# Performance work log

Hardware: AMD Instinct MI355X
Metric: run time of the kernel (lower is better)

## Reference

```python
import jax, jax.numpy as jnp
import numpy as np

B, V, C, A = 32, 48, 24, 6
NC, D, H, OUT = 10000, 128, 128, 167


def setup_inputs() -> dict:
    key = jax.random.key(0)
    ks = jax.random.split(key, 12)
    seqs = jax.random.randint(ks[0], (B, V, C), 0, NC + 1)
    ancestors = jax.random.randint(ks[1], (B, V, C, A), 0, NC + 1)
    length = jax.random.randint(ks[2], (B,), 1, V + 1)
    amask = (jax.random.uniform(ks[3], (B, V, C, A)) < 0.7).astype(jnp.float32)
    amask = amask.at[..., 0].set(1.0)  # first ancestor always valid
    emb = jax.random.normal(ks[4], (NC + 1, D), dtype=jnp.float32) * 0.02
    emb = emb.at[NC].set(0.0)  # padding row is zeros
    w_basic = jax.random.normal(ks[5], (D, 2 * D), dtype=jnp.float32) * (1.0 / np.sqrt(2 * D))
    u_basic_w = jax.random.normal(ks[6], (1, D), dtype=jnp.float32) * (1.0 / np.sqrt(D))
    u_basic_b = jnp.zeros((1,), jnp.float32)
    gru_wih = jax.random.normal(ks[7], (3 * H, D), dtype=jnp.float32) * (1.0 / np.sqrt(H))
    gru_whh = jax.random.normal(ks[8], (3 * H, H), dtype=jnp.float32) * (1.0 / np.sqrt(H))
    gru_bih = jnp.zeros((3 * H,), jnp.float32)
    gru_bhh = jnp.zeros((3 * H,), jnp.float32)
    out_w = jax.random.normal(ks[9], (OUT, H), dtype=jnp.float32) * (1.0 / np.sqrt(H))
    out_b = jnp.zeros((OUT,), jnp.float32)
    return dict(seqs=seqs, ancestors=ancestors, length=length, ancestor_length=amask,
                emb=emb, w_basic=w_basic, u_basic_w=u_basic_w, u_basic_b=u_basic_b,
                gru_wih=gru_wih, gru_whh=gru_whh, gru_bih=gru_bih, gru_bhh=gru_bhh,
                out_w=out_w, out_b=out_b)


def _gram_forward(seqs, ancestors, length, ancestor_length, emb, w_basic,
                  u_basic_w, u_basic_b, gru_wih, gru_whh, gru_bih, gru_bhh,
                  out_w, out_b):
    # gather embeddings
    seqs_e = emb[seqs]            # [B,V,C,D]
    anc_e = emb[ancestors]        # [B,V,C,A,D]
    seqs_rep = jnp.broadcast_to(seqs_e[..., None, :], anc_e.shape)
    # Bahdanau attention: mask applied to concat BEFORE the linear (as in source)
    cat = jnp.concatenate([seqs_rep, anc_e], axis=-1) * ancestor_length[..., None]  # [B,V,C,A,2D]
    hdd = jnp.tanh(jnp.einsum('bvcad,ed->bvcae', cat, w_basic))  # [B,V,C,A,D]
    score = jnp.einsum('bvcad,od->bvcao', hdd, u_basic_w) + u_basic_b  # [B,V,C,A,1]
    # mask_softmax over ancestor axis, faithful to the source (sum==0 -> -1)
    e = jnp.exp(score) * ancestor_length[..., None]
    s = jnp.sum(e, axis=3, keepdims=True)
    s = jnp.where(s == 0, -1.0, s)
    attn = e / s                  # [B,V,C,A,1]
    ctx = jnp.sum(attn * anc_e, axis=3)            # [B,V,C,D] weighted ancestor sum
    x = jnp.tanh(jnp.sum(ctx, axis=2))             # [B,V,D] visit embedding

    # single-layer GRU over visits (valid steps form a prefix, padded tail masked below)
    hsz = gru_whh.shape[1]
    def step(hstate, xt):
        gi = xt @ gru_wih.T + gru_bih              # [B,3H]
        gh = hstate @ gru_whh.T + gru_bhh
        ir, iz, inn = jnp.split(gi, 3, axis=-1)
        hr, hz, hn = jnp.split(gh, 3, axis=-1)
        r = jax.nn.sigmoid(ir + hr)
        z = jax.nn.sigmoid(iz + hz)
        n = jnp.tanh(inn + r * hn)
        hnew = (1.0 - z) * n + z * hstate
        return hnew, hnew
    h0 = jnp.zeros((x.shape[0], hsz), x.dtype)
    _, outs = jax.lax.scan(step, h0, jnp.swapaxes(x, 0, 1))  # [V,B,H]
    outs = jnp.swapaxes(outs, 0, 1)                          # [B,V,H]

    visit_mask = (jnp.arange(x.shape[1])[None, :] < length[:, None]).astype(x.dtype)
    context = jnp.einsum('bv,bvh->bh', visit_mask, outs)     # masked sum over visits
    logit = jax.nn.sigmoid(context @ out_w.T + out_b)        # dropout=eval (identity)
    return logit


def reference(seqs, ancestors, length, ancestor_length, emb, w_basic, u_basic_w,
              u_basic_b, gru_wih, gru_whh, gru_bih, gru_bhh, out_w, out_b):
    return _gram_forward(seqs, ancestors, length, ancestor_length, emb, w_basic,
                         u_basic_w, u_basic_b, gru_wih, gru_whh, gru_bih, gru_bhh,
                         out_w, out_b)
```

## Files before the change

kernel.cpp:

```cpp
#include <hip/hip_runtime.h>

#define BB 32
#define VV 48
#define CC 24
#define AA 6
#define NCODES 10001
#define DD 128
#define HH 128
#define OUTN 167
#define G3 384

typedef float f32x4 __attribute__((ext_vector_type(4)));

__device__ __forceinline__ float fast_tanh(float x) {
    return 1.0f - 2.0f / (1.0f + __expf(2.0f * x));
}
__device__ __forceinline__ float fast_sigmoid(float x) {
    return 1.0f / (1.0f + __expf(-x));
}
__device__ __forceinline__ float dot4(float4 a, float4 b) {
    return a.x * b.x + a.y * b.y + a.z * b.z + a.w * b.w;
}
__device__ __forceinline__ float dot4v(f32x4 a, f32x4 b) {
    return a.x * b.x + a.y * b.y + a.z * b.z + a.w * b.w;
}

__global__ __launch_bounds__(256) void k_precompute(
    const float* __restrict__ emb, const float* __restrict__ w_basic,
    float* __restrict__ P1, float* __restrict__ P2, int nrows)
{
    __shared__ float embs[8][128];
    int row0 = blockIdx.x * 8;
    int t = threadIdx.x;
    for (int i = t; i < 8 * 128; i += 256) {
        int r = i >> 7, d = i & 127;
        int row = row0 + r;
        embs[r][d] = (row < nrows) ? emb[row * 128 + d] : 0.0f;
    }
    __syncthreads();
    int e = t & 127, sel = t >> 7;
    const float* wrow = w_basic + e * 256 + sel * 128;
    float acc[8] = {0, 0, 0, 0, 0, 0, 0, 0};
#pragma unroll 8
    for (int d = 0; d < 128; ++d) {
        float w = wrow[d];
#pragma unroll
        for (int r = 0; r < 8; ++r) acc[r] += embs[r][d] * w;
    }
    float* dst = sel ? P2 : P1;
#pragma unroll
    for (int r = 0; r < 8; ++r) {
        int row = row0 + r;
        if (row < nrows) dst[row * 128 + e] = acc[r];
    }
}

__global__ __launch_bounds__(256) void k_attention(
    const int* __restrict__ seqs, const int* __restrict__ ancestors,
    const float* __restrict__ amask, const float* __restrict__ emb,
    const float* __restrict__ P1, const float* __restrict__ P2,
    const float* __restrict__ u_w, const float* __restrict__ u_b,
    float* __restrict__ x_out)
{
    __shared__ __align__(16) float u_s[128];
    __shared__ float sc_s[144];
    __shared__ float m_s[144];
    __shared__ int   anc_s[144];
    __shared__ float attn_s[144];
    __shared__ float sum_s[24];
    __shared__ float xred[256];
    int bv = blockIdx.x;
    int t = threadIdx.x;
    if (t < 128) u_s[t] = u_w[t];
    __syncthreads();
    float ub = u_b[0];
    int g = t >> 2, l = t & 3;
    for (int p = g; p < CC * AA; p += 64) {
        int c = p / AA, a = p - c * AA;
        int sidx = bv * CC + c;
        int s_code = seqs[sidx];
        int aidx = sidx * AA + a;
        int anc = ancestors[aidx];
        float m = amask[aidx];
        const float4* p14 = (const float4*)(P1 + s_code * 128);
        const float4* p24 = (const float4*)(P2 + anc * 128);
        const float4* u4 = (const float4*)u_s;
        float partial = 0.0f;
        int e4 = l * 8;
#pragma unroll 2
        for (int j = 0; j < 8; ++j) {
            float4 av = p14[e4 + j];
            float4 bv_ = p24[e4 + j];
            float4 uv = u4[e4 + j];
            partial += fast_tanh(m * (av.x + bv_.x)) * uv.x;
            partial += fast_tanh(m * (av.y + bv_.y)) * uv.y;
            partial += fast_tanh(m * (av.z + bv_.z)) * uv.z;
            partial += fast_tanh(m * (av.w + bv_.w)) * uv.w;
        }
        partial += __shfl_xor(partial, 1);
        partial += __shfl_xor(partial, 2);
        if (l == 0) {
            sc_s[p] = partial + ub;
            m_s[p] = m;
            anc_s[p] = anc;
        }
    }
    __syncthreads();
    if (t < CC * AA) attn_s[t] = __expf(sc_s[t]) * m_s[t];
    __syncthreads();
    if (t < CC) {
        float s = 0.0f;
#pragma unroll
        for (int a = 0; a < AA; ++a) s += attn_s[t * AA + a];
        sum_s[t] = (s == 0.0f) ? -1.0f : s;
    }
    __syncthreads();
    if (t < CC * AA) attn_s[t] = attn_s[t] / sum_s[t / AA];
    __syncthreads();
    int e = t & 127, hc = t >> 7;
    float acc = 0.0f;
    for (int c = hc * 12; c < hc * 12 + 12; ++c) {
#pragma unroll
        for (int a = 0; a < AA; ++a) {
            int p = c * AA + a;
            acc += attn_s[p] * emb[anc_s[p] * 128 + e];
        }
    }
    xred[t] = acc;
    __syncthreads();
    if (t < 128) {
        x_out[bv * 128 + t] = fast_tanh(xred[t] + xred[t + 128]);
    }
}

__global__ __launch_bounds__(384, 2) void k_gi(
    const float* __restrict__ x, const float* __restrict__ wih,
    const float* __restrict__ bih, float* __restrict__ gi)
{
    __shared__ __align__(16) float xs[8][128];
    int row0 = blockIdx.x * 8;
    int t = threadIdx.x;
    for (int i = t; i < 8 * 32; i += 384) {
        ((float4*)xs)[i] = ((const float4*)x)[row0 * 32 + i];
    }
    __syncthreads();
    const float4* wrow4 = (const float4*)(wih + t * 128);
    float acc[8] = {0, 0, 0, 0, 0, 0, 0, 0};
#pragma unroll 2
    for (int d4 = 0; d4 < 32; ++d4) {
        float4 wv = wrow4[d4];
#pragma unroll
        for (int r = 0; r < 8; ++r) {
            float4 xv = ((const float4*)xs[r])[d4];
            acc[r] += dot4(xv, wv);
        }
    }
    float bb = bih[t];
#pragma unroll
    for (int r = 0; r < 8; ++r) gi[(row0 + r) * G3 + t] = acc[r] + bb;
}

#define GL4(dst, base, OFF) \
    asm volatile("global_load_dwordx4 %0, %1, off offset:" #OFF \
                 : "=v"(dst) : "v"(base))

__global__ __launch_bounds__(256, 1) void k_gru(
    const float* __restrict__ gi, const float* __restrict__ whh,
    const float* __restrict__ bhh, const int* __restrict__ length,
    const float* __restrict__ out_w, const float* __restrict__ out_b,
    float* __restrict__ out)
{
    __shared__ __align__(16) float hs[2][128];
    __shared__ __align__(16) float ctxs[128];
    int b = blockIdx.x;
    int t = threadIdx.x;
    int o = t >> 1, half = t & 1;

    const f32x4* bwr = (const f32x4*)(whh + o * 128 + half * 64);
    const f32x4* bwz = (const f32x4*)(whh + (128 + o) * 128 + half * 64);
    const f32x4* bwn = (const f32x4*)(whh + (256 + o) * 128 + half * 64);

    f32x4 wr0, wr1, wr2, wr3, wr4, wr5, wr6, wr7,
          wr8, wr9, wr10, wr11, wr12, wr13, wr14, wr15;
    f32x4 wz0, wz1, wz2, wz3, wz4, wz5, wz6, wz7,
          wz8, wz9, wz10, wz11, wz12, wz13, wz14, wz15;
    f32x4 wn0, wn1, wn2, wn3, wn4, wn5, wn6, wn7,
          wn8, wn9, wn10, wn11, wn12, wn13, wn14, wn15;

    GL4(wr0,  bwr, 0);   GL4(wr1,  bwr, 16);  GL4(wr2,  bwr, 32);  GL4(wr3,  bwr, 48);
    GL4(wr4,  bwr, 64);  GL4(wr5,  bwr, 80);  GL4(wr6,  bwr, 96);  GL4(wr7,  bwr, 112);
    GL4(wr8,  bwr, 128); GL4(wr9,  bwr, 144); GL4(wr10, bwr, 160); GL4(wr11, bwr, 176);
    GL4(wr12, bwr, 192); GL4(wr13, bwr, 208); GL4(wr14, bwr, 224); GL4(wr15, bwr, 240);
    GL4(wz0,  bwz, 0);   GL4(wz1,  bwz, 16);  GL4(wz2,  bwz, 32);  GL4(wz3,  bwz, 48);
    GL4(wz4,  bwz, 64);  GL4(wz5,  bwz, 80);  GL4(wz6,  bwz, 96);  GL4(wz7,  bwz, 112);
    GL4(wz8,  bwz, 128); GL4(wz9,  bwz, 144); GL4(wz10, bwz, 160); GL4(wz11, bwz, 176);
    GL4(wz12, bwz, 192); GL4(wz13, bwz, 208); GL4(wz14, bwz, 224); GL4(wz15, bwz, 240);
    GL4(wn0,  bwn, 0);   GL4(wn1,  bwn, 16);  GL4(wn2,  bwn, 32);  GL4(wn3,  bwn, 48);
    GL4(wn4,  bwn, 64);  GL4(wn5,  bwn, 80);  GL4(wn6,  bwn, 96);  GL4(wn7,  bwn, 112);
    GL4(wn8,  bwn, 128); GL4(wn9,  bwn, 144); GL4(wn10, bwn, 160); GL4(wn11, bwn, 176);
    GL4(wn12, bwn, 192); GL4(wn13, bwn, 208); GL4(wn14, bwn, 224); GL4(wn15, bwn, 240);

    float bhr = 0.f, bhz = 0.f, bhn = 0.f;
    if (half == 0) {
        bhr = bhh[o];
        bhz = bhh[128 + o];
        bhn = bhh[256 + o];
    }
    if (t < 128) hs[0][t] = 0.0f;
    int len = length[b];
    float ctx = 0.0f;

    const float* gib = gi + b * VV * G3;
    float aR = 0.f, aZ = 0.f, aN = 0.f;
    float pR = 0.f, pZ = 0.f, pN = 0.f;
    if (half == 0) {
        aR = gib[o];       aZ = gib[128 + o];       aN = gib[256 + o];
        const float* g1 = gib + G3;
        pR = g1[o];        pZ = g1[128 + o];        pN = g1[256 + o];
    }
    asm volatile("s_waitcnt vmcnt(0)" ::: "memory");
    __builtin_amdgcn_sched_barrier(0);
    __syncthreads();

#define STEP2(J, A, B_) do {                                          \
        f32x4 hA = h4[J]; f32x4 hB = h4[J + 1];                       \
        ar0 += dot4v(wr##A, hA);  ar1 += dot4v(wr##B_, hB);           \
        az0 += dot4v(wz##A, hA);  az1 += dot4v(wz##B_, hB);           \
        an0 += dot4v(wn##A, hA);  an1 += dot4v(wn##B_, hB);           \
    } while (0)

    int cur = 0;
    for (int v = 0; v < VV; ++v) {
        float nR = 0.f, nZ = 0.f, nN = 0.f;
        if (half == 0 && v + 2 < VV) {
            const float* g = gib + (v + 2) * G3;
            nR = g[o]; nZ = g[128 + o]; nN = g[256 + o];
        }
        const f32x4* h4 = ((const f32x4*)hs[cur]) + half * 16;
        float ar0 = 0.f, ar1 = 0.f, az0 = 0.f, az1 = 0.f, an0 = 0.f, an1 = 0.f;
        STEP2(0, 0, 1);   STEP2(2, 2, 3);   STEP2(4, 4, 5);   STEP2(6, 6, 7);
        STEP2(8, 8, 9);   STEP2(10, 10, 11); STEP2(12, 12, 13); STEP2(14, 14, 15);
        float ar = ar0 + ar1;
        float az = az0 + az1;
        float an = an0 + an1;
        ar += __shfl_xor(ar, 1);
        az += __shfl_xor(az, 1);
        an += __shfl_xor(an, 1);
        if (half == 0) {
            float r = fast_sigmoid(aR + ar + bhr);
            float z = fast_sigmoid(aZ + az + bhz);
            float n = fast_tanh(aN + r * (an + bhn));
            float hold = hs[cur][o];
            float hnew = (1.0f - z) * n + z * hold;
            hs[cur ^ 1][o] = hnew;
            if (v < len) ctx += hnew;
        }
        aR = pR; aZ = pZ; aN = pN;
        pR = nR; pZ = nZ; pN = nN;
        cur ^= 1;
        __syncthreads();
    }
#undef STEP2

    if (half == 0) ctxs[o] = ctx;
    __syncthreads();
    if (t < OUTN) {
        const float4* w4 = (const float4*)(out_w + t * 128);
        const float4* c4 = (const float4*)ctxs;
        float a0 = 0.f, a1 = 0.f;
#pragma unroll 2
        for (int j = 0; j < 32; j += 2) {
            a0 += dot4(w4[j], c4[j]);
            a1 += dot4(w4[j + 1], c4[j + 1]);
        }
        out[b * OUTN + t] = fast_sigmoid(a0 + a1 + out_b[t]);
    }
}

extern "C" void kernel_launch(void* const* d_in, const int* in_sizes, int n_in,
                              void* d_out, int out_size, void* d_ws, size_t ws_size,
                              hipStream_t stream) {
    const int*   seqs      = (const int*)d_in[0];
    const int*   ancestors = (const int*)d_in[1];
    const int*   length    = (const int*)d_in[2];
    const float* amask     = (const float*)d_in[3];
    const float* emb       = (const float*)d_in[4];
    const float* w_basic   = (const float*)d_in[5];
    const float* u_w       = (const float*)d_in[6];
    const float* u_b       = (const float*)d_in[7];
    const float* wih       = (const float*)d_in[8];
    const float* whh       = (const float*)d_in[9];
    const float* bih       = (const float*)d_in[10];
    const float* bhh       = (const float*)d_in[11];
    const float* out_w     = (const float*)d_in[12];
    const float* out_b     = (const float*)d_in[13];
    float* out = (float*)d_out;

    float* ws = (float*)d_ws;
    float* P1 = ws;
    float* P2 = P1 + NCODES * 128;
    float* x  = P2 + NCODES * 128;
    float* gi = x + BB * VV * 128;

    k_precompute<<<(NCODES + 7) / 8, 256, 0, stream>>>(emb, w_basic, P1, P2, NCODES);
    k_attention<<<BB * VV, 256, 0, stream>>>(seqs, ancestors, amask, emb, P1, P2, u_w, u_b, x);
    k_gi<<<(BB * VV) / 8, 384, 0, stream>>>(x, wih, bih, gi);
    k_gru<<<BB, 256, 0, stream>>>(gi, whh, bhh, length, out_w, out_b, out);
}
```

Baseline: 136.1 us.

## Stage GRU input gates in LDS and pack two batches per GRU block

The GRU kernel now runs two batch rows per 512-thread block and bulk-copies the precomputed input-gate activations into shared memory in two 24-step chunks, replacing the per-step register prefetch from global memory. The k_gi kernel drops its shared-memory staging of x and reads x directly from global, and its occupancy hint is removed. This aims to take global load latency off the serial recurrence, at the cost of 72KB of LDS, a mid-loop reload barrier, and half as many GRU blocks each running twice the threads.

After: 153.7 us. +12.9%, slower.

```diff
diff --git a/kernel.cpp b/kernel.cpp
--- a/kernel.cpp
+++ b/kernel.cpp
@@ -133,26 +133,21 @@
     }
 }
 
-__global__ __launch_bounds__(384, 2) void k_gi(
+__global__ __launch_bounds__(384) void k_gi(
     const float* __restrict__ x, const float* __restrict__ wih,
     const float* __restrict__ bih, float* __restrict__ gi)
 {
-    __shared__ __align__(16) float xs[8][128];
     int row0 = blockIdx.x * 8;
     int t = threadIdx.x;
-    for (int i = t; i < 8 * 32; i += 384) {
-        ((float4*)xs)[i] = ((const float4*)x)[row0 * 32 + i];
-    }
-    __syncthreads();
-    const float4* wrow4 = (const float4*)(wih + t * 128);
-    float acc[8] = {0, 0, 0, 0, 0, 0, 0, 0};
+    const float4* w4 = (const float4*)(wih + t * 128);
+    const float4* x4 = (const float4*)(x + row0 * 128);
+    float acc[8] = {};
 #pragma unroll 2
     for (int d4 = 0; d4 < 32; ++d4) {
-        float4 wv = wrow4[d4];
+        float4 wv = w4[d4];
 #pragma unroll
         for (int r = 0; r < 8; ++r) {
-            float4 xv = ((const float4*)xs[r])[d4];
-            acc[r] += dot4(xv, wv);
+            acc[r] += dot4(x4[r * 32 + d4], wv);
         }
     }
     float bb = bih[t];
@@ -164,17 +159,20 @@
     asm volatile("global_load_dwordx4 %0, %1, off offset:" #OFF \
                  : "=v"(dst) : "v"(base))
 
-__global__ __launch_bounds__(256, 1) void k_gru(
+__global__ __launch_bounds__(512, 1) void k_gru(
     const float* __restrict__ gi, const float* __restrict__ whh,
     const float* __restrict__ bhh, const int* __restrict__ length,
     const float* __restrict__ out_w, const float* __restrict__ out_b,
     float* __restrict__ out)
 {
-    __shared__ __align__(16) float hs[2][128];
-    __shared__ __align__(16) float ctxs[128];
-    int b = blockIdx.x;
+    __shared__ __align__(16) float gl[2][24 * G3];
+    __shared__ __align__(16) float hs[2][2][128];
+    __shared__ __align__(16) float ctxs[2][128];
     int t = threadIdx.x;
-    int o = t >> 1, half = t & 1;
+    int tb = t >> 8;
+    int tt = t & 255;
+    int b = blockIdx.x * 2 + tb;
+    int o = tt >> 1, half = tt & 1;
 
     const f32x4* bwr = (const f32x4*)(whh + o * 128 + half * 64);
     const f32x4* bwz = (const f32x4*)(whh + (128 + o) * 128 + half * 64);
@@ -200,24 +198,23 @@
     GL4(wn8,  bwn, 128); GL4(wn9,  bwn, 144); GL4(wn10, bwn, 160); GL4(wn11, bwn, 176);
     GL4(wn12, bwn, 192); GL4(wn13, bwn, 208); GL4(wn14, bwn, 224); GL4(wn15, bwn, 240);
 
+    const float4* gib4 = (const float4*)(gi + b * VV * G3);
+    {
+        float4* dst = (float4*)gl[tb];
+#pragma unroll
+        for (int i = 0; i < 9; ++i) dst[tt + i * 256] = gib4[tt + i * 256];
+    }
+
     float bhr = 0.f, bhz = 0.f, bhn = 0.f;
     if (half == 0) {
         bhr = bhh[o];
         bhz = bhh[128 + o];
         bhn = bhh[256 + o];
     }
-    if (t < 128) hs[0][t] = 0.0f;
+    if (tt < 128) hs[tb][0][tt] = 0.0f;
     int len = length[b];
     float ctx = 0.0f;
 
-    const float* gib = gi + b * VV * G3;
-    float aR = 0.f, aZ = 0.f, aN = 0.f;
-    float pR = 0.f, pZ = 0.f, pN = 0.f;
-    if (half == 0) {
-        aR = gib[o];       aZ = gib[128 + o];       aN = gib[256 + o];
-        const float* g1 = gib + G3;
-        pR = g1[o];        pZ = g1[128 + o];        pN = g1[256 + o];
-    }
     asm volatile("s_waitcnt vmcnt(0)" ::: "memory");
     __builtin_amdgcn_sched_barrier(0);
     __syncthreads();
@@ -231,14 +228,22 @@
 
     int cur = 0;
     for (int v = 0; v < VV; ++v) {
-        float nR = 0.f, nZ = 0.f, nN = 0.f;
-        if (half == 0 && v + 2 < VV) {
-            const float* g = gib + (v + 2) * G3;
-            nR = g[o]; nZ = g[128 + o]; nN = g[256 + o];
-        }
-        const f32x4* h4 = ((const f32x4*)hs[cur]) + half * 16;
+        if (v == 24) {
+            float4* dst = (float4*)gl[tb];
+            const float4* src = gib4 + 2304;
+#pragma unroll
+            for (int i = 0; i < 9; ++i) dst[tt + i * 256] = src[tt + i * 256];
+            __syncthreads();
+        }
+        int vv = (v >= 24) ? (v - 24) : v;
+        float gir = 0.f, giz = 0.f, gin = 0.f;
+        if (half == 0) {
+            const float* g = gl[tb] + vv * G3;
+            gir = g[o]; giz = g[128 + o]; gin = g[256 + o];
+        }
+        const f32x4* h4 = ((const f32x4*)hs[tb][cur]) + half * 16;
         float ar0 = 0.f, ar1 = 0.f, az0 = 0.f, az1 = 0.f, an0 = 0.f, an1 = 0.f;
-        STEP2(0, 0, 1);   STEP2(2, 2, 3);   STEP2(4, 4, 5);   STEP2(6, 6, 7);
+        STEP2(0, 0, 1);   STEP2(2, 2, 3);    STEP2(4, 4, 5);    STEP2(6, 6, 7);
         STEP2(8, 8, 9);   STEP2(10, 10, 11); STEP2(12, 12, 13); STEP2(14, 14, 15);
         float ar = ar0 + ar1;
         float az = az0 + az1;
@@ -247,33 +252,31 @@
         az += __shfl_xor(az, 1);
         an += __shfl_xor(an, 1);
         if (half == 0) {
-            float r = fast_sigmoid(aR + ar + bhr);
-            float z = fast_sigmoid(aZ + az + bhz);
-            float n = fast_tanh(aN + r * (an + bhn));
-            float hold = hs[cur][o];
+            float r = fast_sigmoid(gir + ar + bhr);
+            float z = fast_sigmoid(giz + az + bhz);
+            float n = fast_tanh(gin + r * (an + bhn));
+            float hold = hs[tb][cur][o];
             float hnew = (1.0f - z) * n + z * hold;
-            hs[cur ^ 1][o] = hnew;
+            hs[tb][cur ^ 1][o] = hnew;
             if (v < len) ctx += hnew;
         }
-        aR = pR; aZ = pZ; aN = pN;
-        pR = nR; pZ = nZ; pN = nN;
         cur ^= 1;
         __syncthreads();
     }
 #undef STEP2
 
-    if (half == 0) ctxs[o] = ctx;
-    __syncthreads();
-    if (t < OUTN) {
-        const float4* w4 = (const float4*)(out_w + t * 128);
-        const float4* c4 = (const float4*)ctxs;
+    if (half == 0) ctxs[tb][o] = ctx;
+    __syncthreads();
+    if (tt < OUTN) {
+        const float4* w4 = (const float4*)(out_w + tt * 128);
+        const float4* c4 = (const float4*)ctxs[tb];
         float a0 = 0.f, a1 = 0.f;
 #pragma unroll 2
         for (int j = 0; j < 32; j += 2) {
             a0 += dot4(w4[j], c4[j]);
             a1 += dot4(w4[j + 1], c4[j + 1]);
         }
-        out[b * OUTN + t] = fast_sigmoid(a0 + a1 + out_b[t]);
+        out[b * OUTN + tt] = fast_sigmoid(a0 + a1 + out_b[tt]);
     }
 }
 
@@ -305,5 +308,5 @@
     k_precompute<<<(NCODES + 7) / 8, 256, 0, stream>>>(emb, w_basic, P1, P2, NCODES);
     k_attention<<<BB * VV, 256, 0, stream>>>(seqs, ancestors, amask, emb, P1, P2, u_w, u_b, x);
     k_gi<<<(BB * VV) / 8, 384, 0, stream>>>(x, wih, bih, gi);
-    k_gru<<<BB, 256, 0, stream>>>(gi, whh, bhh, length, out_w, out_b, out);
-}
+    k_gru<<<BB / 2, 512, 0, stream>>>(gi, whh, bhh, length, out_w, out_b, out);
+}
```
